# Kernel tuning notes

Measured on AMD Instinct MI355X. Metric: run time of the kernel, lower is better.

## Reference

```python
import jax, jax.numpy as jnp
import numpy as np

EMBED_DIM = 2048
HEAD_DIM = 128            # __init__ head_dim arg
HALF = HEAD_DIM // 2      # internal self.head_dim = 64
NH2 = EMBED_DIM // HALF   # 32 q/k heads
H = NH2 // 2              # 16 differential heads
DEPTH = 12
LAMBDA_INIT = 0.8 - 0.6 * float(np.exp(-0.3 * DEPTH))
SCALING = HEAD_DIM ** (-0.5)   # source divides scores by this (== *sqrt(head_dim))
BATCH, SEQ = 1, 2048
EPS = 1e-5


def setup_inputs() -> dict:
    key = jax.random.key(0)
    ks = jax.random.split(key, 10)
    wstd = 0.25 / float(np.sqrt(EMBED_DIM))  # keep logits moderate despite *sqrt(head_dim)
    return {
        "x": jax.random.normal(ks[0], (BATCH, SEQ, EMBED_DIM), jnp.float32),
        "wq": jax.random.normal(ks[1], (EMBED_DIM, EMBED_DIM), jnp.float32) * wstd,
        "wk": jax.random.normal(ks[2], (EMBED_DIM, EMBED_DIM), jnp.float32) * wstd,
        "wv": jax.random.normal(ks[3], (EMBED_DIM, EMBED_DIM), jnp.float32) * wstd,
        "wout": jax.random.normal(ks[4], (EMBED_DIM, EMBED_DIM), jnp.float32) * wstd,
        "lambda_q1": jax.random.normal(ks[5], (HALF,), jnp.float32) * 0.1,
        "lambda_q2": jax.random.normal(ks[6], (HALF,), jnp.float32) * 0.1,
        "lambda_k1": jax.random.normal(ks[7], (HALF,), jnp.float32) * 0.1,
        "lambda_k2": jax.random.normal(ks[8], (HALF,), jnp.float32) * 0.1,
        "subln_weight": jnp.ones((2 * HALF,), jnp.float32),
    }


def _rope_tables(t, dim):
    # precompute_freqs_cis: freqs = 1/theta^(arange(0,dim,2)/dim); angles = outer(t, freqs)
    inv = 1.0 / (10000.0 ** (np.arange(0, dim, 2)[: dim // 2].astype(np.float64) / dim))
    ang = np.outer(np.arange(t), inv)
    return jnp.asarray(np.cos(ang), jnp.float32), jnp.asarray(np.sin(ang), jnp.float32)


def _apply_rope(x, cos, sin):
    # x: [b, t, h, d]; interleaved (even, odd) pairs form complex numbers
    xr, xi = x[..., 0::2], x[..., 1::2]
    c = cos[None, :, None, :]
    s = sin[None, :, None, :]
    out = jnp.stack([xr * c - xi * s, xr * s + xi * c], axis=-1)
    return out.reshape(x.shape)


def reference(x, wq, wk, wv, wout, lambda_q1, lambda_q2, lambda_k1, lambda_k2, subln_weight):
    b, t, e = x.shape
    # nn.Linear(bias=False): y = x @ W^T
    q = (x @ wq.T).reshape(b, t, NH2, HALF)
    k = (x @ wk.T).reshape(b, t, NH2, HALF)
    v = (x @ wv.T).reshape(b, t, H, 2 * HALF)  # intended DIFF-attn layout
    cos, sin = _rope_tables(t, HALF)
    q = _apply_rope(q, cos, sin)
    k = _apply_rope(k, cos, sin)
    q = q.transpose(0, 2, 1, 3)  # [b, 2H, t, HALF]
    k = k.transpose(0, 2, 1, 3)
    v = v.transpose(0, 2, 1, 3)  # [b, H, t, 2*HALF]
    # source: attn_weights = qk / scaling  (scaling = head_dim**-0.5 -> multiply by sqrt(head_dim))
    scores = jnp.einsum('bhtd,bhsd->bhts', q, k) / SCALING
    # default attn_mask = triu(zeros) == all zeros -> no masking applied
    probs = jax.nn.softmax(scores, axis=-1)
    lam1 = jnp.exp(jnp.sum(lambda_q1 * lambda_k1))
    lam2 = jnp.exp(jnp.sum(lambda_q2 * lambda_k2))
    lam = lam1 - lam2 + LAMBDA_INIT
    probs = probs.reshape(b, H, 2, t, t)
    diff = probs[:, :, 0] - lam * probs[:, :, 1]        # [b, H, t, t]
    attn = jnp.einsum('bhts,bhsd->bhtd', diff, v)        # [b, H, t, 2*HALF]
    # RMSNorm(2*HALF, eps=1e-5)
    attn = attn * jax.lax.rsqrt(jnp.mean(attn * attn, axis=-1, keepdims=True) + EPS)
    attn = attn * subln_weight
    attn = attn.transpose(0, 2, 1, 3).reshape(b, t, e)
    return attn @ wout.T
```

## Files before the change

### kernel.cpp

```cpp
#include <hip/hip_runtime.h>
#include <math.h>

#define SEQ 2048
#define EMB 2048

typedef _Float16 f16;
typedef unsigned short ushort_t;
typedef __attribute__((ext_vector_type(2))) _Float16 f16x2;
typedef __attribute__((ext_vector_type(4))) _Float16 f16x4;
typedef __attribute__((ext_vector_type(8))) _Float16 f16x8;
typedef __attribute__((ext_vector_type(4))) float f32x4;
typedef __attribute__((ext_vector_type(8))) short bf16x8;
typedef __attribute__((ext_vector_type(4))) unsigned short us4;
typedef __attribute__((ext_vector_type(8))) unsigned short us8;

__device__ __forceinline__ void gload16(const void* g, void* l) {
  __builtin_amdgcn_global_load_lds((const __attribute__((address_space(1))) unsigned int*)g,
                                   (__attribute__((address_space(3))) unsigned int*)l, 16, 0, 0);
}

__device__ __forceinline__ ushort_t f32_to_bf16(float f) {
  unsigned int u = __builtin_bit_cast(unsigned int, f);
  u += 0x7FFFu + ((u >> 16) & 1u);
  return (ushort_t)(u >> 16);
}

__device__ __forceinline__ unsigned pack2_bf16(float a, float b) {
  unsigned ua = __builtin_bit_cast(unsigned, a) + 0x8000u;
  unsigned ub = __builtin_bit_cast(unsigned, b) + 0x8000u;
  return __builtin_amdgcn_perm(ub, ua, 0x07060302u);
}
__device__ __forceinline__ us4 pack4_bf16(float a, float b, float c, float d) {
  unsigned lo = pack2_bf16(a, b);
  unsigned hi = pack2_bf16(c, d);
  unsigned long long v = ((unsigned long long)hi << 32) | (unsigned long long)lo;
  return __builtin_bit_cast(us4, v);
}

__global__ __launch_bounds__(256) void cvt5_kernel(const float* __restrict__ i0,
                                                   const float* __restrict__ i1,
                                                   const float* __restrict__ i2,
                                                   const float* __restrict__ i3,
                                                   const float* __restrict__ i4,
                                                   f16* __restrict__ o0, f16* __restrict__ o1,
                                                   f16* __restrict__ o2, f16* __restrict__ o3,
                                                   f16* __restrict__ o4) {
  int b = blockIdx.x;
  int z = b >> 12;
  const float* in = (z == 0) ? i0 : (z == 1) ? i1 : (z == 2) ? i2 : (z == 3) ? i3 : i4;
  f16* out = (z == 0) ? o0 : (z == 1) ? o1 : (z == 2) ? o2 : (z == 3) ? o3 : o4;
  int i = ((b & 4095) * 256 + threadIdx.x) * 4;
  f32x4 v = *(const f32x4*)(in + i);
  *(f16x4*)(out + i) = __builtin_convertvector(v, f16x4);
}

__global__ __launch_bounds__(256) void rope_table_kernel(float* __restrict__ cosT,
                                                         float* __restrict__ sinT) {
  int id = blockIdx.x * 256 + threadIdx.x;
  int t = id >> 5, i = id & 31;
  double inv = pow(10000.0, -(double)i / 32.0);
  double ang = (double)t * inv;
  cosT[id] = (float)cos(ang);
  sinT[id] = (float)sin(ang);
}

__global__ __launch_bounds__(256) void rope2_kernel(f16* __restrict__ q, f16* __restrict__ k,
                                                    const float* __restrict__ cosT,
                                                    const float* __restrict__ sinT) {
  f16* x = blockIdx.y ? k : q;
  const float scale = blockIdx.y ? 1.0f : 16.3222307f;
  int id = blockIdx.x * 256 + threadIdx.x;
  int i = id & 31;
  int nh2 = (id >> 5) & 31;
  int t = id >> 10;
  float c = cosT[(t << 5) + i], s = sinT[(t << 5) + i];
  int base = t * EMB + nh2 * 64 + 2 * i;
  f16x2 p = *(f16x2*)(x + base);
  float xr = (float)p.x, xi = (float)p.y;
  f16x2 o;
  o.x = (f16)((xr * c - xi * s) * scale);
  o.y = (f16)((xr * s + xi * c) * scale);
  *(f16x2*)(x + base) = o;
}

__global__ __launch_bounds__(256, 3) void proj_gemm_kernel(
    const f16* __restrict__ A, const f16* __restrict__ B0, const f16* __restrict__ B1,
    const f16* __restrict__ B2, f16* __restrict__ qout, f16* __restrict__ kout,
    ushort_t* __restrict__ vtout) {
  const int z = blockIdx.z;
  const f16* __restrict__ B = (z == 0) ? B0 : ((z == 1) ? B1 : B2);
  __shared__ f16 As[128 * 64];
  __shared__ f16 Bs[128 * 64];
  const int tid = threadIdx.x;
  const int wave = tid >> 6, lane = tid & 63;
  const int l16 = lane & 15, quad = lane >> 4;
  const int wm = (wave >> 1) << 6, wn = (wave & 1) << 6;
  const int bm = blockIdx.y << 7, bn = blockIdx.x << 7;

  const f16* Ag = A + (size_t)(bm + wave * 32 + (lane >> 3)) * EMB + (lane & 7) * 8;
  const f16* Bg = B + (size_t)(bn + wave * 32 + (lane >> 3)) * EMB + (lane & 7) * 8;
  f16* Asl = &As[wave * 2048 + lane * 8];
  f16* Bsl = &Bs[wave * 2048 + lane * 8];

  f32x4 acc[4][4];
#pragma unroll
  for (int i = 0; i < 4; i++)
#pragma unroll
    for (int j = 0; j < 4; j++) acc[i][j] = (f32x4){0.f, 0.f, 0.f, 0.f};

  for (int k0 = 0; k0 < EMB; k0 += 64) {
    __syncthreads();
#pragma unroll
    for (int i = 0; i < 4; i++) gload16(Ag + (size_t)(i * 8) * EMB + k0, Asl + i * 512);
#pragma unroll
    for (int i = 0; i < 4; i++) gload16(Bg + (size_t)(i * 8) * EMB + k0, Bsl + i * 512);
    __syncthreads();
#pragma unroll
    for (int ks = 0; ks < 2; ks++) {
      f16x8 af[4], bf[4];
#pragma unroll
      for (int mi = 0; mi < 4; mi++)
        af[mi] = *(const f16x8*)&As[(wm + mi * 16 + l16) * 64 + ks * 32 + quad * 8];
#pragma unroll
      for (int ni = 0; ni < 4; ni++)
        bf[ni] = *(const f16x8*)&Bs[(wn + ni * 16 + l16) * 64 + ks * 32 + quad * 8];
#pragma unroll
      for (int mi = 0; mi < 4; mi++)
#pragma unroll
        for (int ni = 0; ni < 4; ni++)
          acc[mi][ni] = __builtin_amdgcn_mfma_f32_16x16x32_f16(af[mi], bf[ni], acc[mi][ni], 0, 0, 0);
    }
  }

#pragma unroll
  for (int mi = 0; mi < 4; mi++) {
#pragma unroll
    for (int ni = 0; ni < 4; ni++) {
      int row0 = bm + wm + mi * 16 + quad * 4;
      int col = bn + wn + ni * 16 + l16;
      if (z == 2) {
        us4 o;
#pragma unroll
        for (int rg = 0; rg < 4; rg++) o[rg] = f32_to_bf16(acc[mi][ni][rg]);
        *(us4*)&vtout[(((size_t)(col >> 7)) << 18) + (((size_t)(col & 127)) << 11) + row0] = o;
      } else {
        f16* Co = (z == 0) ? qout : kout;
#pragma unroll
        for (int rg = 0; rg < 4; rg++)
          Co[(size_t)(row0 + rg) * EMB + col] = (f16)acc[mi][ni][rg];
      }
    }
  }
}

__global__ __launch_bounds__(256, 2) void out_gemm_kernel(const f16* __restrict__ A,
                                                          const f16* __restrict__ B,
                                                          float* __restrict__ C) {
  __shared__ f16 As[128 * 64];
  __shared__ f16 Bs[64 * 64];
  const int tid = threadIdx.x;
  const int wave = tid >> 6, lane = tid & 63;
  const int l16 = lane & 15, quad = lane >> 4;
  const int wm = (wave >> 1) << 6, wn = (wave & 1) << 5;
  const int bm = blockIdx.y << 7, bn = blockIdx.x << 6;

  const f16* Ag = A + (size_t)(bm + wave * 32 + (lane >> 3)) * EMB + (lane & 7) * 8;
  const f16* Bg = B + (size_t)(bn + wave * 16 + (lane >> 3)) * EMB + (lane & 7) * 8;
  f16* Asl = &As[wave * 2048 + lane * 8];
  f16* Bsl = &Bs[wave * 1024 + lane * 8];

  f32x4 acc[4][2];
#pragma unroll
  for (int i = 0; i < 4; i++)
#pragma unroll
    for (int j = 0; j < 2; j++) acc[i][j] = (f32x4){0.f, 0.f, 0.f, 0.f};

  for (int k0 = 0; k0 < EMB; k0 += 64) {
    __syncthreads();
#pragma unroll
    for (int i = 0; i < 4; i++) gload16(Ag + (size_t)(i * 8) * EMB + k0, Asl + i * 512);
#pragma unroll
    for (int i = 0; i < 2; i++) gload16(Bg + (size_t)(i * 8) * EMB + k0, Bsl + i * 512);
    __syncthreads();
#pragma unroll
    for (int ks = 0; ks < 2; ks++) {
      f16x8 af[4], bf[2];
#pragma unroll
      for (int mi = 0; mi < 4; mi++)
        af[mi] = *(const f16x8*)&As[(wm + mi * 16 + l16) * 64 + ks * 32 + quad * 8];
#pragma unroll
      for (int ni = 0; ni < 2; ni++)
        bf[ni] = *(const f16x8*)&Bs[(wn + ni * 16 + l16) * 64 + ks * 32 + quad * 8];
#pragma unroll
      for (int mi = 0; mi < 4; mi++)
#pragma unroll
        for (int ni = 0; ni < 2; ni++)
          acc[mi][ni] = __builtin_amdgcn_mfma_f32_16x16x32_f16(af[mi], bf[ni], acc[mi][ni], 0, 0, 0);
    }
  }

#pragma unroll
  for (int mi = 0; mi < 4; mi++) {
#pragma unroll
    for (int ni = 0; ni < 2; ni++) {
      int row0 = bm + wm + mi * 16 + quad * 4;
      int col = bn + wn + ni * 16 + l16;
#pragma unroll
      for (int rg = 0; rg < 4; rg++)
        C[(size_t)(row0 + rg) * EMB + col] = acc[mi][ni][rg];
    }
  }
}

__global__ __launch_bounds__(256, 2) void diff_attn_mfma(
    const f16* __restrict__ qb, const f16* __restrict__ kb, const ushort_t* __restrict__ vbT,
    const float* __restrict__ lq1, const float* __restrict__ lq2,
    const float* __restrict__ lk1, const float* __restrict__ lk2,
    const float* __restrict__ subw, f16* __restrict__ attnb) {
  const int h = blockIdx.y;
  const int qblk = blockIdx.x;
  const int tid = threadIdx.x;
  const int wave = tid >> 6, lane = tid & 63;
  const int l16 = lane & 15, quad = lane >> 4;

  __shared__ f16 Ks[2][16 * 512];
  __shared__ ushort_t Vt[2][16 * 512];
  __shared__ ushort_t Ps[4][2][2][512];

  const int qrowbase = qblk * 64 + wave * 16;
  f16x8 qf[2][2];
#pragma unroll
  for (int hh = 0; hh < 2; hh++)
#pragma unroll
    for (int kt = 0; kt < 2; kt++)
      qf[hh][kt] = *(const f16x8*)(qb + (size_t)(qrowbase + l16) * EMB + h * 128 + hh * 64 +
                                   kt * 32 + quad * 8);

  f32x4 O[2][8];
#pragma unroll
  for (int o = 0; o < 2; o++)
#pragma unroll
    for (int mt = 0; mt < 8; mt++) O[o][mt] = (f32x4){0.f, 0.f, 0.f, 0.f};
  float lsum[2] = {0.f, 0.f};

  const f16* kgp = kb + (size_t)(wave * 16 + (lane >> 2)) * EMB + h * 128 + (lane & 3) * 32;
  const ushort_t* vgp =
      vbT + (((size_t)h) << 18) + (((size_t)(wave * 32 + (lane >> 1))) << 11) + (lane & 1) * 32;
  int koff[4], voff[4];
#pragma unroll
  for (int j = 0; j < 4; j++) {
    int Tk = ((lane & 3) >> 1) * 8 + ((lane & 3) & 1) * 4 + wave;
    koff[j] = Tk * 512 + (j * 16 + (lane >> 2)) * 8;
    int Tv = (lane & 1) * 8 + wave * 2 + (lane >> 5);
    voff[j] = Tv * 512 + (j * 16 + ((lane >> 1) & 15)) * 8;
  }

  {
    f16x8 kreg[4];
    us8 vreg[4];
#pragma unroll
    for (int j = 0; j < 4; j++) kreg[j] = *(const f16x8*)(kgp + j * 8);
#pragma unroll
    for (int j = 0; j < 4; j++) vreg[j] = *(const us8*)(vgp + j * 8);
#pragma unroll
    for (int j = 0; j < 4; j++) *(f16x8*)&Ks[0][koff[j]] = kreg[j];
#pragma unroll
    for (int j = 0; j < 4; j++) *(us8*)&Vt[0][voff[j]] = vreg[j];
    __syncthreads();
  }

  auto step = [&](const f16* KsC, const ushort_t* VtC, f16* KsN, ushort_t* VtN, int it) {
    const int nxt = (it + 1 < 32) ? (it + 1) * 64 : 0;
    f16x8 kreg[4];
    us8 vreg[4];
#pragma unroll
    for (int j = 0; j < 4; j++) kreg[j] = *(const f16x8*)(kgp + (size_t)nxt * EMB + j * 8);
#pragma unroll
    for (int j = 0; j < 4; j++) vreg[j] = *(const us8*)(vgp + nxt + j * 8);

#pragma unroll
    for (int hh = 0; hh < 2; hh++) {
#pragma unroll
      for (int mt = 0; mt < 4; mt++) {
        f16x8 ka0 = *(const f16x8*)&KsC[(hh * 8 + mt) * 512 + lane * 8];
        f16x8 ka1 = *(const f16x8*)&KsC[(hh * 8 + 4 + mt) * 512 + lane * 8];
        f32x4 c = (f32x4){0.f, 0.f, 0.f, 0.f};
        c = __builtin_amdgcn_mfma_f32_16x16x32_f16(ka0, qf[hh][0], c, 0, 0, 0);
        c = __builtin_amdgcn_mfma_f32_16x16x32_f16(ka1, qf[hh][1], c, 0, 0, 0);
        float p0 = __builtin_exp2f(c[0] - 28.8539008f);
        float p1 = __builtin_exp2f(c[1] - 28.8539008f);
        float p2 = __builtin_exp2f(c[2] - 28.8539008f);
        float p3 = __builtin_exp2f(c[3] - 28.8539008f);
        lsum[hh] += (p0 + p1) + (p2 + p3);
        us4 pb = pack4_bf16(p0, p1, p2, p3);
        int poff = (((mt & 1) * 2 + (quad >> 1)) * 16 + l16) * 8 + (quad & 1) * 4;
        *(us4*)&Ps[wave][hh][mt >> 1][poff] = pb;
      }
    }

#pragma unroll
    for (int kk = 0; kk < 2; kk++) {
      bf16x8 pf0 = *(const bf16x8*)&Ps[wave][0][kk][lane * 8];
      bf16x8 pf1 = *(const bf16x8*)&Ps[wave][1][kk][lane * 8];
#pragma unroll
      for (int mt = 0; mt < 8; mt++) {
        bf16x8 va = *(const bf16x8*)&VtC[(kk * 8 + mt) * 512 + lane * 8];
        O[0][mt] = __builtin_amdgcn_mfma_f32_16x16x32_bf16(va, pf0, O[0][mt], 0, 0, 0);
        O[1][mt] = __builtin_amdgcn_mfma_f32_16x16x32_bf16(va, pf1, O[1][mt], 0, 0, 0);
      }
    }

#pragma unroll
    for (int j = 0; j < 4; j++) *(f16x8*)&KsN[koff[j]] = kreg[j];
#pragma unroll
    for (int j = 0; j < 4; j++) *(us8*)&VtN[voff[j]] = vreg[j];
    __syncthreads();
  };

  for (int it = 0; it < 32; it += 2) {
    step(Ks[0], Vt[0], Ks[1], Vt[1], it);
    step(Ks[1], Vt[1], Ks[0], Vt[0], it + 1);
  }

  float d1 = 0.f, d2 = 0.f;
  for (int i = 0; i < 64; i++) {
    d1 += lq1[i] * lk1[i];
    d2 += lq2[i] * lk2[i];
  }
  const float lam = __expf(d1) - __expf(d2) + 0.783605767f;

  float s0 = lsum[0];
  s0 += __shfl_xor(s0, 16);
  s0 += __shfl_xor(s0, 32);
  float s1 = lsum[1];
  s1 += __shfl_xor(s1, 16);
  s1 += __shfl_xor(s1, 32);
  const float inv0 = 1.f / s0;
  const float inv1 = lam / s1;

  f32x4 swv[8];
#pragma unroll
  for (int mt = 0; mt < 8; mt++) swv[mt] = *(const f32x4*)(subw + mt * 16 + quad * 4);

  float a[8][4];
  float ms = 0.f;
#pragma unroll
  for (int mt = 0; mt < 8; mt++)
#pragma unroll
    for (int rg = 0; rg < 4; rg++) {
      float v = O[0][mt][rg] * inv0 - O[1][mt][rg] * inv1;
      a[mt][rg] = v;
      ms += v * v;
    }
  ms += __shfl_xor(ms, 16);
  ms += __shfl_xor(ms, 32);
  const float rms = rsqrtf(ms * (1.f / 128.f) + 1e-5f);
  const int t_g = qrowbase + l16;
#pragma unroll
  for (int mt = 0; mt < 8; mt++) {
    f16x4 o;
#pragma unroll
    for (int rg = 0; rg < 4; rg++) o[rg] = (f16)(a[mt][rg] * rms * swv[mt][rg]);
    *(f16x4*)(attnb + (size_t)t_g * EMB + h * 128 + mt * 16 + quad * 4) = o;
  }
}

extern "C" void kernel_launch(void* const* d_in, const int* in_sizes, int n_in,
                              void* d_out, int out_size, void* d_ws, size_t ws_size,
                              hipStream_t stream) {
  const float* x    = (const float*)d_in[0];
  const float* wq   = (const float*)d_in[1];
  const float* wk   = (const float*)d_in[2];
  const float* wv   = (const float*)d_in[3];
  const float* wout = (const float*)d_in[4];
  const float* lq1  = (const float*)d_in[5];
  const float* lq2  = (const float*)d_in[6];
  const float* lk1  = (const float*)d_in[7];
  const float* lk2  = (const float*)d_in[8];
  const float* subw = (const float*)d_in[9];
  float* out = (float*)d_out;

  char* ws = (char*)d_ws;
  const size_t MB = 1024 * 1024;
  f16* xb    = (f16*)(ws + 0 * MB);
  f16* wqb   = (f16*)(ws + 8 * MB);
  f16* wkb   = (f16*)(ws + 16 * MB);
  f16* wvb   = (f16*)(ws + 24 * MB);
  f16* woutb = (f16*)(ws + 32 * MB);
  f16* qb    = (f16*)(ws + 40 * MB);
  f16* kb    = (f16*)(ws + 48 * MB);
  ushort_t* vbT = (ushort_t*)(ws + 56 * MB);
  f16* attnb = (f16*)(ws + 64 * MB);
  float* cosT = (float*)(ws + 72 * MB);
  float* sinT = (float*)(ws + 72 * MB + 262144);

  dim3 b256(256);
  cvt5_kernel<<<5 * 4096, b256, 0, stream>>>(x, wq, wk, wv, wout, xb, wqb, wkb, wvb, woutb);
  rope_table_kernel<<<256, b256, 0, stream>>>(cosT, sinT);

  proj_gemm_kernel<<<dim3(16, 16, 3), b256, 0, stream>>>(xb, wqb, wkb, wvb, qb, kb, vbT);

  rope2_kernel<<<dim3(8192, 2), b256, 0, stream>>>(qb, kb, cosT, sinT);

  diff_attn_mfma<<<dim3(32, 16), b256, 0, stream>>>(qb, kb, vbT, lq1, lq2, lk1, lk2, subw, attnb);

  out_gemm_kernel<<<dim3(32, 16), b256, 0, stream>>>(attnb, woutb, out);
}
```

Baseline: 321.0 us.

## Swizzle GEMM LDS tiles, pre-tile V globally, and restructure diff-attention wave split

Both GEMMs move to a K-step of 32 with an XOR-swizzled LDS layout, aimed at avoiding bank conflicts, at the cost of twice as many barriers. The V projection now writes V already in the MFMA fragment tile order, so the attention kernel loads V fragments straight from global memory and no longer stages V in LDS. The attention kernel assigns each wave one sub-head and 32 query rows instead of both sub-heads and 16 rows, combines the two sub-heads through an LDS buffer in the epilogue, swizzles K in LDS, and raises occupancy to 3 blocks per CU. Loading V from global memory inside the loop relies on cache and memory latency being hidden, and the smaller GEMM tiles add synchronisation overhead.

```diff
diff --git a/kernel.cpp b/kernel.cpp
--- a/kernel.cpp
+++ b/kernel.cpp
@@ -89,18 +89,27 @@
     ushort_t* __restrict__ vtout) {
   const int z = blockIdx.z;
   const f16* __restrict__ B = (z == 0) ? B0 : ((z == 1) ? B1 : B2);
-  __shared__ f16 As[128 * 64];
-  __shared__ f16 Bs[128 * 64];
+  __shared__ f16 As[128 * 32];
+  __shared__ f16 Bs[128 * 32];
   const int tid = threadIdx.x;
   const int wave = tid >> 6, lane = tid & 63;
   const int l16 = lane & 15, quad = lane >> 4;
   const int wm = (wave >> 1) << 6, wn = (wave & 1) << 6;
   const int bm = blockIdx.y << 7, bn = blockIdx.x << 7;
 
-  const f16* Ag = A + (size_t)(bm + wave * 32 + (lane >> 3)) * EMB + (lane & 7) * 8;
-  const f16* Bg = B + (size_t)(bn + wave * 32 + (lane >> 3)) * EMB + (lane & 7) * 8;
-  f16* Asl = &As[wave * 2048 + lane * 8];
-  f16* Bsl = &Bs[wave * 2048 + lane * 8];
+  const int swg = ((lane & 3) ^ ((lane >> 3) & 3)) * 8;
+  const f16* Ag = A + (size_t)(bm + wave * 32 + (lane >> 2)) * EMB + swg;
+  const f16* Bg = B + (size_t)(bn + wave * 32 + (lane >> 2)) * EMB + swg;
+  f16* Asl = &As[wave * 1024 + lane * 8];
+  f16* Bsl = &Bs[wave * 1024 + lane * 8];
+
+  const int swr = (quad ^ ((l16 >> 1) & 3)) * 8;
+  int aoff[4], boff[4];
+#pragma unroll
+  for (int i = 0; i < 4; i++) {
+    aoff[i] = (wm + i * 16 + l16) * 32 + swr;
+    boff[i] = (wn + i * 16 + l16) * 32 + swr;
+  }
 
   f32x4 acc[4][4];
 #pragma unroll
@@ -108,28 +117,23 @@
 #pragma unroll
     for (int j = 0; j < 4; j++) acc[i][j] = (f32x4){0.f, 0.f, 0.f, 0.f};
 
-  for (int k0 = 0; k0 < EMB; k0 += 64) {
-    __syncthreads();
-#pragma unroll
-    for (int i = 0; i < 4; i++) gload16(Ag + (size_t)(i * 8) * EMB + k0, Asl + i * 512);
-#pragma unroll
-    for (int i = 0; i < 4; i++) gload16(Bg + (size_t)(i * 8) * EMB + k0, Bsl + i * 512);
-    __syncthreads();
-#pragma unroll
-    for (int ks = 0; ks < 2; ks++) {
-      f16x8 af[4], bf[4];
-#pragma unroll
-      for (int mi = 0; mi < 4; mi++)
-        af[mi] = *(const f16x8*)&As[(wm + mi * 16 + l16) * 64 + ks * 32 + quad * 8];
+  for (int k0 = 0; k0 < EMB; k0 += 32) {
+    __syncthreads();
+    gload16(Ag + k0, Asl);
+    gload16(Ag + (size_t)16 * EMB + k0, Asl + 512);
+    gload16(Bg + k0, Bsl);
+    gload16(Bg + (size_t)16 * EMB + k0, Bsl + 512);
+    __syncthreads();
+    f16x8 af[4], bf[4];
+#pragma unroll
+    for (int mi = 0; mi < 4; mi++) af[mi] = *(const f16x8*)&As[aoff[mi]];
+#pragma unroll
+    for (int ni = 0; ni < 4; ni++) bf[ni] = *(const f16x8*)&Bs[boff[ni]];
+#pragma unroll
+    for (int mi = 0; mi < 4; mi++)
 #pragma unroll
       for (int ni = 0; ni < 4; ni++)
-        bf[ni] = *(const f16x8*)&Bs[(wn + ni * 16 + l16) * 64 + ks * 32 + quad * 8];
-#pragma unroll
-      for (int mi = 0; mi < 4; mi++)
-#pragma unroll
-        for (int ni = 0; ni < 4; ni++)
-          acc[mi][ni] = __builtin_amdgcn_mfma_f32_16x16x32_f16(af[mi], bf[ni], acc[mi][ni], 0, 0, 0);
-    }
+        acc[mi][ni] = __builtin_amdgcn_mfma_f32_16x16x32_f16(af[mi], bf[ni], acc[mi][ni], 0, 0, 0);
   }
 
 #pragma unroll
@@ -142,7 +146,10 @@
         us4 o;
 #pragma unroll
         for (int rg = 0; rg < 4; rg++) o[rg] = f32_to_bf16(acc[mi][ni][rg]);
-        *(us4*)&vtout[(((size_t)(col >> 7)) << 18) + (((size_t)(col & 127)) << 11) + row0] = o;
+        int hidx = col >> 7, d = col & 127, t = row0;
+        size_t idx = ((size_t)((hidx * 32 + (t >> 6)) * 16 + ((t >> 5) & 1) * 8 + (d >> 4))) * 512 +
+                     (((t >> 3) & 3) * 16 + (d & 15)) * 8 + (t & 7);
+        *(us4*)&vtout[idx] = o;
       } else {
         f16* Co = (z == 0) ? qout : kout;
 #pragma unroll
@@ -156,18 +163,26 @@
 __global__ __launch_bounds__(256, 2) void out_gemm_kernel(const f16* __restrict__ A,
                                                           const f16* __restrict__ B,
                                                           float* __restrict__ C) {
-  __shared__ f16 As[128 * 64];
-  __shared__ f16 Bs[64 * 64];
+  __shared__ f16 As[128 * 32];
+  __shared__ f16 Bs[64 * 32];
   const int tid = threadIdx.x;
   const int wave = tid >> 6, lane = tid & 63;
   const int l16 = lane & 15, quad = lane >> 4;
   const int wm = (wave >> 1) << 6, wn = (wave & 1) << 5;
   const int bm = blockIdx.y << 7, bn = blockIdx.x << 6;
 
-  const f16* Ag = A + (size_t)(bm + wave * 32 + (lane >> 3)) * EMB + (lane & 7) * 8;
-  const f16* Bg = B + (size_t)(bn + wave * 16 + (lane >> 3)) * EMB + (lane & 7) * 8;
-  f16* Asl = &As[wave * 2048 + lane * 8];
-  f16* Bsl = &Bs[wave * 1024 + lane * 8];
+  const int swg = ((lane & 3) ^ ((lane >> 3) & 3)) * 8;
+  const f16* Ag = A + (size_t)(bm + wave * 32 + (lane >> 2)) * EMB + swg;
+  const f16* Bg = B + (size_t)(bn + wave * 16 + (lane >> 2)) * EMB + swg;
+  f16* Asl = &As[wave * 1024 + lane * 8];
+  f16* Bsl = &Bs[wave * 512 + lane * 8];
+
+  const int swr = (quad ^ ((l16 >> 1) & 3)) * 8;
+  int aoff[4], boff[2];
+#pragma unroll
+  for (int i = 0; i < 4; i++) aoff[i] = (wm + i * 16 + l16) * 32 + swr;
+#pragma unroll
+  for (int i = 0; i < 2; i++) boff[i] = (wn + i * 16 + l16) * 32 + swr;
 
   f32x4 acc[4][2];
 #pragma unroll
@@ -175,28 +190,22 @@
 #pragma unroll
     for (int j = 0; j < 2; j++) acc[i][j] = (f32x4){0.f, 0.f, 0.f, 0.f};
 
-  for (int k0 = 0; k0 < EMB; k0 += 64) {
-    __syncthreads();
-#pragma unroll
-    for (int i = 0; i < 4; i++) gload16(Ag + (size_t)(i * 8) * EMB + k0, Asl + i * 512);
-#pragma unroll
-    for (int i = 0; i < 2; i++) gload16(Bg + (size_t)(i * 8) * EMB + k0, Bsl + i * 512);
-    __syncthreads();
-#pragma unroll
-    for (int ks = 0; ks < 2; ks++) {
-      f16x8 af[4], bf[2];
-#pragma unroll
-      for (int mi = 0; mi < 4; mi++)
-        af[mi] = *(const f16x8*)&As[(wm + mi * 16 + l16) * 64 + ks * 32 + quad * 8];
+  for (int k0 = 0; k0 < EMB; k0 += 32) {
+    __syncthreads();
+    gload16(Ag + k0, Asl);
+    gload16(Ag + (size_t)16 * EMB + k0, Asl + 512);
+    gload16(Bg + k0, Bsl);
+    __syncthreads();
+    f16x8 af[4], bf[2];
+#pragma unroll
+    for (int mi = 0; mi < 4; mi++) af[mi] = *(const f16x8*)&As[aoff[mi]];
+#pragma unroll
+    for (int ni = 0; ni < 2; ni++) bf[ni] = *(const f16x8*)&Bs[boff[ni]];
+#pragma unroll
+    for (int mi = 0; mi < 4; mi++)
 #pragma unroll
       for (int ni = 0; ni < 2; ni++)
-        bf[ni] = *(const f16x8*)&Bs[(wn + ni * 16 + l16) * 64 + ks * 32 + quad * 8];
-#pragma unroll
-      for (int mi = 0; mi < 4; mi++)
-#pragma unroll
-        for (int ni = 0; ni < 2; ni++)
-          acc[mi][ni] = __builtin_amdgcn_mfma_f32_16x16x32_f16(af[mi], bf[ni], acc[mi][ni], 0, 0, 0);
-    }
+        acc[mi][ni] = __builtin_amdgcn_mfma_f32_16x16x32_f16(af[mi], bf[ni], acc[mi][ni], 0, 0, 0);
   }
 
 #pragma unroll
@@ -212,114 +221,127 @@
   }
 }
 
-__global__ __launch_bounds__(256, 2) void diff_attn_mfma(
+__global__ __launch_bounds__(256, 3) void diff_attn_v3(
     const f16* __restrict__ qb, const f16* __restrict__ kb, const ushort_t* __restrict__ vbT,
     const float* __restrict__ lq1, const float* __restrict__ lq2,
     const float* __restrict__ lk1, const float* __restrict__ lk2,
     const float* __restrict__ subw, f16* __restrict__ attnb) {
-  const int h = blockIdx.y;
-  const int qblk = blockIdx.x;
+  const int h = blockIdx.x;
+  const int qblk = blockIdx.y;
   const int tid = threadIdx.x;
   const int wave = tid >> 6, lane = tid & 63;
   const int l16 = lane & 15, quad = lane >> 4;
-
-  __shared__ f16 Ks[2][16 * 512];
-  __shared__ ushort_t Vt[2][16 * 512];
-  __shared__ ushort_t Ps[4][2][2][512];
-
-  const int qrowbase = qblk * 64 + wave * 16;
+  const int hh = wave >> 1, qs = wave & 1;
+
+  __shared__ f16 Ks[2][8192];
+  __shared__ ushort_t Ps[4][4][512];
+
+  const int qrow0 = qblk * 64 + qs * 32;
   f16x8 qf[2][2];
 #pragma unroll
-  for (int hh = 0; hh < 2; hh++)
+  for (int nt = 0; nt < 2; nt++)
 #pragma unroll
     for (int kt = 0; kt < 2; kt++)
-      qf[hh][kt] = *(const f16x8*)(qb + (size_t)(qrowbase + l16) * EMB + h * 128 + hh * 64 +
-                                   kt * 32 + quad * 8);
-
-  f32x4 O[2][8];
-#pragma unroll
-  for (int o = 0; o < 2; o++)
-#pragma unroll
-    for (int mt = 0; mt < 8; mt++) O[o][mt] = (f32x4){0.f, 0.f, 0.f, 0.f};
+      qf[nt][kt] = *(const f16x8*)(qb + (size_t)(qrow0 + nt * 16 + l16) * EMB + h * 128 +
+                                   hh * 64 + kt * 32 + quad * 8);
+
+  f32x4 O[8][2];
+#pragma unroll
+  for (int mt = 0; mt < 8; mt++)
+#pragma unroll
+    for (int nt = 0; nt < 2; nt++) O[mt][nt] = (f32x4){0.f, 0.f, 0.f, 0.f};
   float lsum[2] = {0.f, 0.f};
 
   const f16* kgp = kb + (size_t)(wave * 16 + (lane >> 2)) * EMB + h * 128 + (lane & 3) * 32;
-  const ushort_t* vgp =
-      vbT + (((size_t)h) << 18) + (((size_t)(wave * 32 + (lane >> 1))) << 11) + (lane & 1) * 32;
-  int koff[4], voff[4];
+  int koff[4];
 #pragma unroll
   for (int j = 0; j < 4; j++) {
-    int Tk = ((lane & 3) >> 1) * 8 + ((lane & 3) & 1) * 4 + wave;
-    koff[j] = Tk * 512 + (j * 16 + (lane >> 2)) * 8;
-    int Tv = (lane & 1) * 8 + wave * 2 + (lane >> 5);
-    voff[j] = Tv * 512 + (j * 16 + ((lane >> 1) & 15)) * 8;
-  }
+    int d8 = (lane & 3) * 4 + j;
+    int T = (d8 >> 3) * 8 + ((d8 >> 2) & 1) * 4 + wave;
+    int ch = (d8 & 3) * 16 + (lane >> 2);
+    koff[j] = T * 512 + ((ch ^ (T & 7)) * 8);
+  }
+  int kro[2][4];
+#pragma unroll
+  for (int kt = 0; kt < 2; kt++)
+#pragma unroll
+    for (int mt = 0; mt < 4; mt++) {
+      int T = hh * 8 + kt * 4 + mt;
+      kro[kt][mt] = T * 512 + ((lane ^ (T & 7)) * 8);
+    }
+
+  const ushort_t* vg = vbT + ((size_t)h << 18) + lane * 8;
 
   {
     f16x8 kreg[4];
-    us8 vreg[4];
 #pragma unroll
     for (int j = 0; j < 4; j++) kreg[j] = *(const f16x8*)(kgp + j * 8);
 #pragma unroll
-    for (int j = 0; j < 4; j++) vreg[j] = *(const us8*)(vgp + j * 8);
-#pragma unroll
     for (int j = 0; j < 4; j++) *(f16x8*)&Ks[0][koff[j]] = kreg[j];
-#pragma unroll
-    for (int j = 0; j < 4; j++) *(us8*)&Vt[0][voff[j]] = vreg[j];
-    __syncthreads();
-  }
-
-  auto step = [&](const f16* KsC, const ushort_t* VtC, f16* KsN, ushort_t* VtN, int it) {
+    __syncthreads();
+  }
+
+  auto step = [&](const f16* KsC, f16* KsN, int it) {
+    const size_t vit = (size_t)(it * 16) * 512;
+    us8 va0[8];
+#pragma unroll
+    for (int mt = 0; mt < 8; mt++) va0[mt] = *(const us8*)(vg + vit + mt * 512);
     const int nxt = (it + 1 < 32) ? (it + 1) * 64 : 0;
     f16x8 kreg[4];
-    us8 vreg[4];
 #pragma unroll
     for (int j = 0; j < 4; j++) kreg[j] = *(const f16x8*)(kgp + (size_t)nxt * EMB + j * 8);
-#pragma unroll
-    for (int j = 0; j < 4; j++) vreg[j] = *(const us8*)(vgp + nxt + j * 8);
-
-#pragma unroll
-    for (int hh = 0; hh < 2; hh++) {
-#pragma unroll
-      for (int mt = 0; mt < 4; mt++) {
-        f16x8 ka0 = *(const f16x8*)&KsC[(hh * 8 + mt) * 512 + lane * 8];
-        f16x8 ka1 = *(const f16x8*)&KsC[(hh * 8 + 4 + mt) * 512 + lane * 8];
+
+#pragma unroll
+    for (int mt = 0; mt < 4; mt++) {
+      f16x8 ka0 = *(const f16x8*)&KsC[kro[0][mt]];
+      f16x8 ka1 = *(const f16x8*)&KsC[kro[1][mt]];
+#pragma unroll
+      for (int nt = 0; nt < 2; nt++) {
         f32x4 c = (f32x4){0.f, 0.f, 0.f, 0.f};
-        c = __builtin_amdgcn_mfma_f32_16x16x32_f16(ka0, qf[hh][0], c, 0, 0, 0);
-        c = __builtin_amdgcn_mfma_f32_16x16x32_f16(ka1, qf[hh][1], c, 0, 0, 0);
+        c = __builtin_amdgcn_mfma_f32_16x16x32_f16(ka0, qf[nt][0], c, 0, 0, 0);
+        c = __builtin_amdgcn_mfma_f32_16x16x32_f16(ka1, qf[nt][1], c, 0, 0, 0);
         float p0 = __builtin_exp2f(c[0] - 28.8539008f);
         float p1 = __builtin_exp2f(c[1] - 28.8539008f);
         float p2 = __builtin_exp2f(c[2] - 28.8539008f);
         float p3 = __builtin_exp2f(c[3] - 28.8539008f);
-        lsum[hh] += (p0 + p1) + (p2 + p3);
+        lsum[nt] += (p0 + p1) + (p2 + p3);
         us4 pb = pack4_bf16(p0, p1, p2, p3);
         int poff = (((mt & 1) * 2 + (quad >> 1)) * 16 + l16) * 8 + (quad & 1) * 4;
-        *(us4*)&Ps[wave][hh][mt >> 1][poff] = pb;
-      }
-    }
-
-#pragma unroll
-    for (int kk = 0; kk < 2; kk++) {
-      bf16x8 pf0 = *(const bf16x8*)&Ps[wave][0][kk][lane * 8];
-      bf16x8 pf1 = *(const bf16x8*)&Ps[wave][1][kk][lane * 8];
+        *(us4*)&Ps[wave][nt * 2 + (mt >> 1)][poff] = pb;
+      }
+    }
+    us8 va1[8];
+#pragma unroll
+    for (int mt = 0; mt < 8; mt++) va1[mt] = *(const us8*)(vg + vit + (8 + mt) * 512);
+
+    {
+      bf16x8 pf0 = *(const bf16x8*)&Ps[wave][0][lane * 8];
+      bf16x8 pf1 = *(const bf16x8*)&Ps[wave][2][lane * 8];
 #pragma unroll
       for (int mt = 0; mt < 8; mt++) {
-        bf16x8 va = *(const bf16x8*)&VtC[(kk * 8 + mt) * 512 + lane * 8];
-        O[0][mt] = __builtin_amdgcn_mfma_f32_16x16x32_bf16(va, pf0, O[0][mt], 0, 0, 0);
-        O[1][mt] = __builtin_amdgcn_mfma_f32_16x16x32_bf16(va, pf1, O[1][mt], 0, 0, 0);
-      }
-    }
-
+        bf16x8 va = __builtin_bit_cast(bf16x8, va0[mt]);
+        O[mt][0] = __builtin_amdgcn_mfma_f32_16x16x32_bf16(va, pf0, O[mt][0], 0, 0, 0);
+        O[mt][1] = __builtin_amdgcn_mfma_f32_16x16x32_bf16(va, pf1, O[mt][1], 0, 0, 0);
+      }
+    }
+    {
+      bf16x8 pf0 = *(const bf16x8*)&Ps[wave][1][lane * 8];
+      bf16x8 pf1 = *(const bf16x8*)&Ps[wave][3][lane * 8];
+#pragma unroll
+      for (int mt = 0; mt < 8; mt++) {
+        bf16x8 va = __builtin_bit_cast(bf16x8, va1[mt]);
+        O[mt][0] = __builtin_amdgcn_mfma_f32_16x16x32_bf16(va, pf0, O[mt][0], 0, 0, 0);
+        O[mt][1] = __builtin_amdgcn_mfma_f32_16x16x32_bf16(va, pf1, O[mt][1], 0, 0, 0);
+      }
+    }
 #pragma unroll
     for (int j = 0; j < 4; j++) *(f16x8*)&KsN[koff[j]] = kreg[j];
-#pragma unroll
-    for (int j = 0; j < 4; j++) *(us8*)&VtN[voff[j]] = vreg[j];
     __syncthreads();
   };
 
   for (int it = 0; it < 32; it += 2) {
-    step(Ks[0], Vt[0], Ks[1], Vt[1], it);
-    step(Ks[1], Vt[1], Ks[0], Vt[0], it + 1);
+    step(Ks[0][0] ? Ks[0] : Ks[0], Ks[1], it);
+    step(Ks[1], Ks[0], it + 1);
   }
 
   float d1 = 0.f, d2 = 0.f;
@@ -328,40 +350,56 @@
     d2 += lq2[i] * lk2[i];
   }
   const float lam = __expf(d1) - __expf(d2) + 0.783605767f;
-
-  float s0 = lsum[0];
-  s0 += __shfl_xor(s0, 16);
-  s0 += __shfl_xor(s0, 32);
-  float s1 = lsum[1];
-  s1 += __shfl_xor(s1, 16);
-  s1 += __shfl_xor(s1, 32);
-  const float inv0 = 1.f / s0;
-  const float inv1 = lam / s1;
-
-  f32x4 swv[8];
-#pragma unroll
-  for (int mt = 0; mt < 8; mt++) swv[mt] = *(const f32x4*)(subw + mt * 16 + quad * 4);
-
-  float a[8][4];
-  float ms = 0.f;
-#pragma unroll
-  for (int mt = 0; mt < 8; mt++)
-#pragma unroll
-    for (int rg = 0; rg < 4; rg++) {
-      float v = O[0][mt][rg] * inv0 - O[1][mt][rg] * inv1;
-      a[mt][rg] = v;
-      ms += v * v;
-    }
-  ms += __shfl_xor(ms, 16);
-  ms += __shfl_xor(ms, 32);
-  const float rms = rsqrtf(ms * (1.f / 128.f) + 1e-5f);
-  const int t_g = qrowbase + l16;
-#pragma unroll
-  for (int mt = 0; mt < 8; mt++) {
-    f16x4 o;
-#pragma unroll
-    for (int rg = 0; rg < 4; rg++) o[rg] = (f16)(a[mt][rg] * rms * swv[mt][rg]);
-    *(f16x4*)(attnb + (size_t)t_g * EMB + h * 128 + mt * 16 + quad * 4) = o;
+  float inv[2];
+#pragma unroll
+  for (int nt = 0; nt < 2; nt++) {
+    float s = lsum[nt];
+    s += __shfl_xor(s, 16);
+    s += __shfl_xor(s, 32);
+    inv[nt] = (hh == 0) ? (1.f / s) : (lam / s);
+  }
+
+  float* Obuf = (float*)&Ks[0][0];
+  if (hh == 1) {
+#pragma unroll
+    for (int mt = 0; mt < 8; mt++)
+#pragma unroll
+      for (int nt = 0; nt < 2; nt++) {
+        f32x4 v = O[mt][nt] * inv[nt];
+        *(f32x4*)&Obuf[qs * 4096 + (nt * 8 + mt) * 256 + lane * 4] = v;
+      }
+  }
+  __syncthreads();
+  if (hh == 0) {
+    f32x4 swv[8];
+#pragma unroll
+    for (int mt = 0; mt < 8; mt++) swv[mt] = *(const f32x4*)(subw + mt * 16 + quad * 4);
+#pragma unroll
+    for (int nt = 0; nt < 2; nt++) {
+      float a[8][4];
+      float ms = 0.f;
+#pragma unroll
+      for (int mt = 0; mt < 8; mt++) {
+        f32x4 o1 = *(const f32x4*)&Obuf[qs * 4096 + (nt * 8 + mt) * 256 + lane * 4];
+#pragma unroll
+        for (int rg = 0; rg < 4; rg++) {
+          float v = O[mt][nt][rg] * inv[nt] - o1[rg];
+          a[mt][rg] = v;
+          ms += v * v;
+        }
+      }
+      ms += __shfl_xor(ms, 16);
+      ms += __shfl_xor(ms, 32);
+      const float rms = rsqrtf(ms * (1.f / 128.f) + 1e-5f);
+      const int t_g = qrow0 + nt * 16 + l16;
+#pragma unroll
+      for (int mt = 0; mt < 8; mt++) {
+        f16x4 o;
+#pragma unroll
+        for (int rg = 0; rg < 4; rg++) o[rg] = (f16)(a[mt][rg] * rms * swv[mt][rg]);
+        *(f16x4*)(attnb + (size_t)t_g * EMB + h * 128 + mt * 16 + quad * 4) = o;
+      }
+    }
   }
 }
 
@@ -402,7 +440,7 @@
 
   rope2_kernel<<<dim3(8192, 2), b256, 0, stream>>>(qb, kb, cosT, sinT);
 
-  diff_attn_mfma<<<dim3(32, 16), b256, 0, stream>>>(qb, kb, vbT, lq1, lq2, lk1, lk2, subw, attnb);
+  diff_attn_v3<<<dim3(16, 32), b256, 0, stream>>>(qb, kb, vbT, lq1, lq2, lk1, lk2, subw, attnb);
 
   out_gemm_kernel<<<dim3(32, 16), b256, 0, stream>>>(attnb, woutb, out);
 }
```

Measured after the change: 397.6 us. 1.24x slower.
